# Kernel tuning notes

Measured on AMD Instinct MI355X. Metric: run time of the kernel, lower is better.

The kernel has to match this reference:

```python
import jax, jax.numpy as jnp
import numpy as np
import math

DIM = 896
NH = 8
HD = DIM // NH  # 112
B, T, KA_RAW, KT = 64, 8, 64, 512
KA = KA_RAW + 1  # adapter tokens + p conditioning token


def rope_cos_sin(L, hd):
    inv = 1.0 / (10000.0 ** (jnp.arange(0, hd, 2, dtype=jnp.float32) / hd))
    freqs = jnp.arange(L, dtype=jnp.float32)[:, None] * inv[None, :]  # (L, hd/2)
    emb = jnp.concatenate([freqs, freqs], axis=-1)  # (L, hd)
    return jnp.cos(emb), jnp.sin(emb)


def rotate_half(x):
    # interleaved rotation, faithful to the torch code
    x1 = x[..., ::2]
    x2 = x[..., 1::2]
    return jnp.stack((-x2, x1), axis=-1).reshape(x.shape)


def rope_apply(t, cos, sin):
    # cos/sin: (L, hd) broadcast over (B, H, L, hd)
    return t * cos + rotate_half(t) * sin


def heads(t):
    Bb, L, _ = t.shape
    return t.reshape(Bb, L, NH, HD).transpose(0, 2, 1, 3)  # (B, H, L, hd)


def setup_inputs() -> dict:
    key = jax.random.key(0)
    ks = jax.random.split(key, 32)
    s = 0.02
    d = {
        'x': jax.random.normal(ks[0], (B, T, DIM), jnp.float32),
        'h_a': jax.random.normal(ks[1], (B, KA_RAW, DIM), jnp.float32),
        'h_t': jax.random.normal(ks[2], (B, KT, DIM), jnp.float32),
        'p': jax.random.normal(ks[3], (B, 1, DIM), jnp.float32),
    }
    names = ['Wq', 'Wks', 'Wvs', 'Wka', 'Wva', 'Wkt', 'Wvt', 'Wo', 'Wf']
    for i, n in enumerate(names):
        d[n] = s * jax.random.normal(ks[4 + i], (DIM, DIM), jnp.float32)
        d['b' + n[1:]] = s * jax.random.normal(ks[16 + i], (DIM,), jnp.float32)
    d['gate'] = jnp.full((1,), 0.1, jnp.float32)  # nonzero so task branch is active
    d['ln_g'] = jnp.ones((DIM,), jnp.float32)
    d['ln_b'] = jnp.zeros((DIM,), jnp.float32)
    return d


def reference(x, h_a, h_t, p,
              Wq, bq, Wks, bks, Wvs, bvs, Wka, bka, Wva, bva,
              Wkt, bkt, Wvt, bvt, Wo, bo, Wf, bf,
              gate, ln_g, ln_b):
    ratio_g = jnp.tanh(gate)  # (1,)
    h_ad = jnp.concatenate([h_a, p], axis=1)  # (B, KA, C)

    q = heads(x @ Wq + bq)            # (B,H,T,hd)
    k_s = heads(x @ Wks + bks)
    v_s = heads(x @ Wvs + bvs)
    k_a = heads(h_ad @ Wka + bka)     # (B,H,KA,hd)
    v_a = heads(h_ad @ Wva + bva)
    k_t = heads(h_t @ Wkt + bkt)      # (B,H,KT,hd)
    v_t = heads(h_t @ Wvt + bvt)

    cos_m, sin_m = rope_cos_sin(T, HD)
    q = rope_apply(q, cos_m, sin_m)
    k_s = rope_apply(k_s, cos_m, sin_m)
    cos_a, sin_a = rope_cos_sin(KA, HD)
    k_a = rope_apply(k_a, cos_a, sin_a)
    cos_t, sin_t = rope_cos_sin(KT, HD)
    k_t = rope_apply(k_t, cos_t, sin_t)

    s_self = jnp.einsum('bhtd,bhkd->bhtk', q, k_s)
    s_ad = jnp.einsum('bhtd,bhkd->bhtk', q, k_a)
    s_task = jnp.einsum('bhtd,bhkd->bhtk', q, k_t) * ratio_g
    scores = jnp.concatenate([s_self, s_ad, s_task], axis=-1) / math.sqrt(HD)
    w = jax.nn.softmax(scores, axis=-1)  # (B,H,T,T+KA+KT)

    v = jnp.concatenate([v_s, v_a, v_t], axis=2)  # (B,H,T+KA+KT,hd)
    out = jnp.einsum('bhtk,bhkd->bhtd', w, v)
    out = out.transpose(0, 2, 1, 3).reshape(x.shape)  # (B,T,C)
    out = out @ Wo + bo

    y = out + x
    mu = jnp.mean(y, axis=-1, keepdims=True)
    var = jnp.var(y, axis=-1, keepdims=True)
    yn = (y - mu) / jnp.sqrt(var + 1e-5) * ln_g + ln_b
    return jax.nn.relu(yn @ Wf + bf)
```

## Files before the change

### kernel.cpp

```cpp
#include <hip/hip_runtime.h>
#include <hip/hip_bf16.h>
#include <math.h>

#define DIM 896
#define DD  (DIM * DIM)
#define NH 8
#define HD 112
#define BB 64
#define TT 8
#define KA 65
#define KAPAD 4224
#define KT 512
#define NKEYS (TT + KA + KT)

#define EPI_NONE  0
#define EPI_ROPE  1
#define EPI_RESID 2
#define EPI_RELU  3

#define NEG_L2_10K_OVER_56 (-0.2373327285062406f)

#ifndef __has_builtin
#define __has_builtin(x) 0
#endif
#if __has_builtin(__builtin_amdgcn_global_load_lds)
#define HAS_GLL 1
#else
#define HAS_GLL 0
#endif

typedef __attribute__((ext_vector_type(8))) short bf16x8_t;
typedef __attribute__((ext_vector_type(4))) float f32x4_t;

__device__ __forceinline__ short f2bf(float f) {
  unsigned u = __float_as_uint(f);
  u += 0x7fffu + ((u >> 16) & 1u);
  return (short)(u >> 16);
}
__device__ __forceinline__ float bf2f(short s) {
  return __uint_as_float(((unsigned)(unsigned short)s) << 16);
}
__device__ __forceinline__ unsigned cvt_pk_bf16(float lo, float hi) {
  unsigned r;
  asm("v_cvt_pk_bf16_f32 %0, %1, %2" : "=v"(r) : "v"(lo), "v"(hi));
  return r;
}

struct W9 { const float* w[9]; };

__global__ __launch_bounds__(256) void wtrans(W9 ws, short* __restrict__ Wt)
{
  __shared__ float t[32][33];
  const float* W = ws.w[blockIdx.z];
  short* dst = Wt + (size_t)blockIdx.z * DD;
  const int bx = blockIdx.x, by = blockIdx.y;
  const int tx = threadIdx.x & 31, ty = threadIdx.x >> 5;
#pragma unroll
  for (int i = 0; i < 4; ++i)
    t[ty + i * 8][tx] = W[(size_t)(by * 32 + ty + i * 8) * DIM + bx * 32 + tx];
  __syncthreads();
#pragma unroll
  for (int i = 0; i < 4; ++i)
    dst[(size_t)(bx * 32 + ty + i * 8) * DIM + by * 32 + tx] = f2bf(t[tx][ty + i * 8]);
}

__global__ __launch_bounds__(256) void build_had(
    const float* __restrict__ h_a, const float* __restrict__ p,
    short* __restrict__ had)
{
  const int i = blockIdx.x * 256 + threadIdx.x;
  const int total = KAPAD * DIM / 8;
  if (i >= total) return;
  const int c = (i % 112) * 8;
  const int row = i / 112;
  bf16x8_t o;
  if (row >= BB * KA) {
#pragma unroll
    for (int j = 0; j < 8; ++j) o[j] = 0;
  } else {
    const int b = row / KA, j = row % KA;
    const float* src = (j < KA - 1) ? h_a + ((size_t)b * (KA - 1) + j) * DIM + c
                                    : p + (size_t)b * DIM + c;
    const float4 a = *(const float4*)src;
    const float4 d = *(const float4*)(src + 4);
    o[0] = f2bf(a.x); o[1] = f2bf(a.y); o[2] = f2bf(a.z); o[3] = f2bf(a.w);
    o[4] = f2bf(d.x); o[5] = f2bf(d.y); o[6] = f2bf(d.z); o[7] = f2bf(d.w);
  }
  ((bf16x8_t*)had)[i] = o;
}

struct EpiCfg {
  const float* bias[3];
  float* outF[3];
  short* outB[3];
  const float* resid;
  int epi[3];
  int pos_mod[3];
  int row_off;
  int hm[3];
  int hm_L[3];
  int hm_ltot[3];
  int swz;
};

template <bool AF32>
__global__ __launch_bounds__(256) void gemm_bf16(
    const short* __restrict__ A, const float* __restrict__ Af,
    const short* __restrict__ Wt, EpiCfg cfg)
{
  __shared__ __align__(16) short As[128 * 32];
  __shared__ __align__(16) short Bs[128 * 32];
  const int tid = threadIdx.x;
  const int wave = tid >> 6, lane = tid & 63;

  int bx = blockIdx.x, by = blockIdx.y;
  if (cfg.swz) {
    const int nx = gridDim.x;
    const int bid = blockIdx.x + blockIdx.y * nx;
    const int xcd = bid & 7, ixd = bid >> 3;
    const int rpx = gridDim.y >> 3;
    bx = ixd % nx;
    by = xcd * rpx + ixd / nx;
  }
  const int sub = bx / 7;
  const int col0 = (bx % 7) * 128;
  const int row0 = by * 128;
  const int wm = wave >> 1, wn = wave & 1;
  const int lm = lane & 15, lq = lane >> 4;

  const int sm = lane >> 2, sk = (lane & 3) * 8;
  const short* Ag0 = A + (size_t)(row0 + wave * 32 + sm) * DIM + sk;
  const short* Ag1 = Ag0 + (size_t)16 * DIM;
  const short* Wg0 = Wt + (size_t)(sub * DIM + col0 + wave * 32 + sm) * DIM + sk;
  const short* Wg1 = Wg0 + (size_t)16 * DIM;

  const int am = tid >> 2, ako = (tid & 3) * 8;
  const float* af0 = nullptr;
  const float* af1 = nullptr;
  float4 c0a, c0b, c1a, c1b;
  if constexpr (AF32) {
    af0 = Af + (size_t)(row0 + am) * DIM + ako;
    af1 = Af + (size_t)(row0 + 64 + am) * DIM + ako;
    c0a = *(const float4*)(af0);
    c0b = *(const float4*)(af0 + 4);
    c1a = *(const float4*)(af1);
    c1b = *(const float4*)(af1 + 4);
  }

  f32x4_t acc[4][4];
#pragma unroll
  for (int i = 0; i < 4; ++i)
#pragma unroll
    for (int j = 0; j < 4; ++j) acc[i][j] = (f32x4_t){0.f, 0.f, 0.f, 0.f};

  for (int k0 = 0; k0 < DIM; k0 += 32) {
    __syncthreads();
    if constexpr (AF32) {
      const int kn = (k0 + 32 < DIM) ? (k0 + 32) : 0;
      const float4 n0a = *(const float4*)(af0 + kn);
      const float4 n0b = *(const float4*)(af0 + kn + 4);
      const float4 n1a = *(const float4*)(af1 + kn);
      const float4 n1b = *(const float4*)(af1 + kn + 4);
      uint4 w;
      w.x = cvt_pk_bf16(c0a.x, c0a.y);
      w.y = cvt_pk_bf16(c0a.z, c0a.w);
      w.z = cvt_pk_bf16(c0b.x, c0b.y);
      w.w = cvt_pk_bf16(c0b.z, c0b.w);
      *(uint4*)&As[tid * 8] = w;
      w.x = cvt_pk_bf16(c1a.x, c1a.y);
      w.y = cvt_pk_bf16(c1a.z, c1a.w);
      w.z = cvt_pk_bf16(c1b.x, c1b.y);
      w.w = cvt_pk_bf16(c1b.z, c1b.w);
      *(uint4*)&As[(tid + 256) * 8] = w;
      c0a = n0a; c0b = n0b; c1a = n1a; c1b = n1b;
    }
#if HAS_GLL
    if constexpr (!AF32) {
      __builtin_amdgcn_global_load_lds(
          (const __attribute__((address_space(1))) unsigned*)(Ag0 + k0),
          (__attribute__((address_space(3))) unsigned*)&As[(wave * 32) * 32], 16, 0, 0);
      __builtin_amdgcn_global_load_lds(
          (const __attribute__((address_space(1))) unsigned*)(Ag1 + k0),
          (__attribute__((address_space(3))) unsigned*)&As[(wave * 32 + 16) * 32], 16, 0, 0);
    }
    __builtin_amdgcn_global_load_lds(
        (const __attribute__((address_space(1))) unsigned*)(Wg0 + k0),
        (__attribute__((address_space(3))) unsigned*)&Bs[(wave * 32) * 32], 16, 0, 0);
    __builtin_amdgcn_global_load_lds(
        (const __attribute__((address_space(1))) unsigned*)(Wg1 + k0),
        (__attribute__((address_space(3))) unsigned*)&Bs[(wave * 32 + 16) * 32], 16, 0, 0);
#else
    {
      const int m = tid >> 1, kh = (tid & 1) * 16;
      if constexpr (!AF32) {
        *(bf16x8_t*)&As[m * 32 + kh] =
            *(const bf16x8_t*)(A + (size_t)(row0 + m) * DIM + k0 + kh);
        *(bf16x8_t*)&As[m * 32 + kh + 8] =
            *(const bf16x8_t*)(A + (size_t)(row0 + m) * DIM + k0 + kh + 8);
      }
      *(bf16x8_t*)&Bs[m * 32 + kh] =
          *(const bf16x8_t*)(Wt + (size_t)(sub * DIM + col0 + m) * DIM + k0 + kh);
      *(bf16x8_t*)&Bs[m * 32 + kh + 8] =
          *(const bf16x8_t*)(Wt + (size_t)(sub * DIM + col0 + m) * DIM + k0 + kh + 8);
    }
#endif
    __syncthreads();

    bf16x8_t af[4], bfr[4];
#pragma unroll
    for (int t = 0; t < 4; ++t)
      af[t] = *(const bf16x8_t*)&As[(wm * 64 + t * 16 + lm) * 32 + lq * 8];
#pragma unroll
    for (int t = 0; t < 4; ++t)
      bfr[t] = *(const bf16x8_t*)&Bs[(wn * 64 + t * 16 + lm) * 32 + lq * 8];
#pragma unroll
    for (int tm = 0; tm < 4; ++tm)
#pragma unroll
      for (int tn = 0; tn < 4; ++tn)
        acc[tm][tn] = __builtin_amdgcn_mfma_f32_16x16x32_bf16(
            af[tm], bfr[tn], acc[tm][tn], 0, 0, 0);
  }

  const float* bias = cfg.bias[sub];
  float* outF = cfg.outF[sub];
  short* outB = cfg.outB[sub];
  const int epi = cfg.epi[sub], pm = cfg.pos_mod[sub];
  const int hm = cfg.hm[sub];
  const int L = cfg.hm_L[sub], ltot = cfg.hm_ltot[sub];
  int gb[4][4], gl[4][4];
  if (hm) {
#pragma unroll
    for (int tm = 0; tm < 4; ++tm) {
      const int g = cfg.row_off + row0 + wm * 64 + tm * 16 + lq * 4;
      int bq2 = g / L;
      int l = g - bq2 * L;
#pragma unroll
      for (int r = 0; r < 4; ++r) {
        gb[tm][r] = bq2; gl[tm][r] = l;
        if (++l == L) { l = 0; ++bq2; }
      }
    }
  }
#pragma unroll
  for (int tn = 0; tn < 4; ++tn) {
    const int col = col0 + wn * 64 + tn * 16 + lm;
    const float bv = bias[col];
    int hcol = 0, dcol = 0;
    if (hm) { hcol = col / HD; dcol = col - hcol * HD; }
    float fr = 0.f, sgn = 0.f;
    if (epi == EPI_ROPE) {
      const int d0 = col % HD;
      fr = exp2f((float)(d0 % 56) * NEG_L2_10K_OVER_56);
      sgn = (d0 & 1) ? 1.f : -1.f;
    }
#pragma unroll
    for (int tm = 0; tm < 4; ++tm) {
#pragma unroll
      for (int r = 0; r < 4; ++r) {
        const int grow = cfg.row_off + row0 + wm * 64 + tm * 16 + lq * 4 + r;
        float v = acc[tm][tn][r] + bv;
        if (epi == EPI_ROPE) {
          const float prt = __shfl_xor(v, 1);
          const int pos = hm ? gl[tm][r] : (grow % pm);
          float s, c;
          __sincosf((float)pos * fr, &s, &c);
          v = v * c + sgn * prt * s;
        } else if (epi == EPI_RESID) {
          v += cfg.resid[(size_t)grow * DIM + col];
        } else if (epi == EPI_RELU) {
          v = fmaxf(v, 0.f);
        }
        if (hm) {
          if (gb[tm][r] < BB)
            outB[((size_t)(gb[tm][r] * NH + hcol) * ltot + gl[tm][r]) * HD + dcol] =
                f2bf(v);
        } else if (outB) {
          outB[(size_t)grow * DIM + col] = f2bf(v);
        } else {
          outF[(size_t)grow * DIM + col] = v;
        }
      }
    }
  }
}

#define SCP 10

__global__ __launch_bounds__(1024, 8) void attn_kernel(
    const short* __restrict__ q, const short* __restrict__ kall,
    const short* __restrict__ vall, const float* __restrict__ gate,
    short* __restrict__ out)
{
  __shared__ __align__(16) float qs[TT * HD];
  __shared__ __align__(16) float sc[NKEYS * SCP];
  __shared__ float red[TT * TT * HD];
  __shared__ float isum[TT];
  const int tid = threadIdx.x;
  const int bh = blockIdx.x;
  const float scale = 0.09449111825230681f;
  const float rg = tanhf(gate[0]);

  if (tid < TT * HD) qs[tid] = bf2f(q[(size_t)bh * (TT * HD) + tid]);
  __syncthreads();

  if (tid < NKEYS) {
    const int k = tid;
    const short* kp = kall + ((size_t)bh * NKEYS + k) * HD;
    float dot[TT] = {};
    for (int d8 = 0; d8 < HD; d8 += 8) {
      const bf16x8_t kv8 = *(const bf16x8_t*)(kp + d8);
      float kf[8];
#pragma unroll
      for (int j = 0; j < 8; ++j) kf[j] = bf2f(kv8[j]);
#pragma unroll
      for (int t = 0; t < TT; ++t) {
        const float4 qa = *(const float4*)&qs[t * HD + d8];
        const float4 qb4 = *(const float4*)&qs[t * HD + d8 + 4];
        dot[t] = fmaf(qa.x, kf[0], dot[t]);
        dot[t] = fmaf(qa.y, kf[1], dot[t]);
        dot[t] = fmaf(qa.z, kf[2], dot[t]);
        dot[t] = fmaf(qa.w, kf[3], dot[t]);
        dot[t] = fmaf(qb4.x, kf[4], dot[t]);
        dot[t] = fmaf(qb4.y, kf[5], dot[t]);
        dot[t] = fmaf(qb4.z, kf[6], dot[t]);
        dot[t] = fmaf(qb4.w, kf[7], dot[t]);
      }
    }
    const float s = (k >= TT + KA) ? scale * rg : scale;
#pragma unroll
    for (int t = 0; t < TT; ++t) sc[k * SCP + t] = dot[t] * s;
  }
  __syncthreads();

  const int wave = tid >> 6, lane = tid & 63;
  if (wave < TT) {
    const int t = wave;
    float m = -1e30f;
    for (int k = lane; k < NKEYS; k += 64) m = fmaxf(m, sc[k * SCP + t]);
#pragma unroll
    for (int o = 32; o >= 1; o >>= 1) m = fmaxf(m, __shfl_xor(m, o));
    float sum = 0.f;
    for (int k = lane; k < NKEYS; k += 64) {
      const float e = expf(sc[k * SCP + t] - m);
      sc[k * SCP + t] = e;
      sum += e;
    }
#pragma unroll
    for (int o = 32; o >= 1; o >>= 1) sum += __shfl_xor(sum, o);
    if (lane == 0) isum[t] = 1.f / sum;
  }
  __syncthreads();

  if (tid < TT * HD) {
    const int g = tid / HD, d = tid - (tid / HD) * HD;
    const int kb = (g * NKEYS) / TT, ke = ((g + 1) * NKEYS) / TT;
    const short* vp = vall + (size_t)bh * (NKEYS * HD) + d;
    float acc[TT] = {};
    for (int k = kb; k < ke; ++k) {
      const float vv = bf2f(vp[(size_t)k * HD]);
      const float2 s0 = *(const float2*)&sc[k * SCP];
      const float2 s1 = *(const float2*)&sc[k * SCP + 2];
      const float2 s2 = *(const float2*)&sc[k * SCP + 4];
      const float2 s3 = *(const float2*)&sc[k * SCP + 6];
      acc[0] = fmaf(s0.x, vv, acc[0]);
      acc[1] = fmaf(s0.y, vv, acc[1]);
      acc[2] = fmaf(s1.x, vv, acc[2]);
      acc[3] = fmaf(s1.y, vv, acc[3]);
      acc[4] = fmaf(s2.x, vv, acc[4]);
      acc[5] = fmaf(s2.y, vv, acc[5]);
      acc[6] = fmaf(s3.x, vv, acc[6]);
      acc[7] = fmaf(s3.y, vv, acc[7]);
    }
#pragma unroll
    for (int t = 0; t < TT; ++t) red[(g * TT + t) * HD + d] = acc[t];
  }
  __syncthreads();

  if (tid < TT * HD) {
    const int t = tid / HD, d = tid - (tid / HD) * HD;
    float a = 0.f;
#pragma unroll
    for (int g = 0; g < TT; ++g) a += red[(g * TT + t) * HD + d];
    out[((size_t)(bh >> 3) * TT + t) * DIM + (bh & 7) * HD + d] = f2bf(a * isum[t]);
  }
}

__global__ __launch_bounds__(256) void ln_kernel(
    const float* __restrict__ y, const float* __restrict__ g,
    const float* __restrict__ beta, short* __restrict__ yn)
{
  __shared__ float s1[4], s2[4];
  const int r = blockIdx.x, tid = threadIdx.x;
  const float* row = y + (size_t)r * DIM;
  float sum = 0.f, sq = 0.f;
  for (int c = tid; c < DIM; c += 256) {
    const float v = row[c];
    sum += v;
    sq = fmaf(v, v, sq);
  }
#pragma unroll
  for (int o = 32; o >= 1; o >>= 1) {
    sum += __shfl_xor(sum, o);
    sq  += __shfl_xor(sq, o);
  }
  const int wave = tid >> 6, lane = tid & 63;
  if (lane == 0) { s1[wave] = sum; s2[wave] = sq; }
  __syncthreads();
  sum = s1[0] + s1[1] + s1[2] + s1[3];
  sq  = s2[0] + s2[1] + s2[2] + s2[3];
  const float mu = sum / DIM;
  const float var = sq / DIM - mu * mu;
  const float rstd = 1.f / sqrtf(var + 1e-5f);
  for (int c = tid; c < DIM; c += 256)
    yn[(size_t)r * DIM + c] = f2bf((row[c] - mu) * rstd * g[c] + beta[c]);
}

extern "C" void kernel_launch(void* const* d_in, const int* in_sizes, int n_in,
                              void* d_out, int out_size, void* d_ws, size_t ws_size,
                              hipStream_t stream)
{
  const float* x   = (const float*)d_in[0];
  const float* h_a = (const float*)d_in[1];
  const float* h_t = (const float*)d_in[2];
  const float* p   = (const float*)d_in[3];
  const float* Wq  = (const float*)d_in[4];  const float* bq  = (const float*)d_in[5];
  const float* Wks = (const float*)d_in[6];  const float* bks = (const float*)d_in[7];
  const float* Wvs = (const float*)d_in[8];  const float* bvs = (const float*)d_in[9];
  const float* Wka = (const float*)d_in[10]; const float* bka = (const float*)d_in[11];
  const float* Wva = (const float*)d_in[12]; const float* bva = (const float*)d_in[13];
  const float* Wkt = (const float*)d_in[14]; const float* bkt = (const float*)d_in[15];
  const float* Wvt = (const float*)d_in[16]; const float* bvt = (const float*)d_in[17];
  const float* Wo  = (const float*)d_in[18]; const float* bo  = (const float*)d_in[19];
  const float* Wf  = (const float*)d_in[20]; const float* bf_ = (const float*)d_in[21];
  const float* gate = (const float*)d_in[22];
  const float* ln_g = (const float*)d_in[23];
  const float* ln_b = (const float*)d_in[24];

  const size_t SZ_HAD = (size_t)KAPAD * DIM * 2;
  const size_t SZ_SM  = (size_t)BB * TT * DIM * 2;
  const size_t SZ_KV  = (size_t)BB * NH * NKEYS * HD * 2;
  const size_t SZ_WT  = (size_t)9 * DD * 2;
  const size_t needed = SZ_HAD + SZ_SM * 3 + SZ_KV * 2 + SZ_WT
                        + (size_t)BB * TT * DIM * 4;
  if (ws_size < needed) return;

  char* wsp = (char*)d_ws;
  short* hadb = (short*)wsp; wsp += SZ_HAD;
  short* qb   = (short*)wsp; wsp += SZ_SM;
  short* kall = (short*)wsp; wsp += SZ_KV;
  short* vall = (short*)wsp; wsp += SZ_KV;
  short* WtA  = (short*)wsp; wsp += SZ_WT;
  short* attn_outb = (short*)wsp; wsp += SZ_SM;
  float* yb   = (float*)wsp; wsp += (size_t)BB * TT * DIM * 4;
  short* ynb  = (short*)wsp; wsp += SZ_SM;

  dim3 blk(256);

  W9 w9; const float* Ws[9] = {Wq, Wks, Wvs, Wka, Wva, Wkt, Wvt, Wo, Wf};
  for (int i = 0; i < 9; ++i) w9.w[i] = Ws[i];
  wtrans<<<dim3(28, 28, 9), blk, 0, stream>>>(w9, WtA);

  build_had<<<(KAPAD * DIM / 8 + 255) / 256, blk, 0, stream>>>(h_a, p, hadb);

  {
    EpiCfg c = {};
    c.bias[0] = bq;  c.outB[0] = qb;   c.epi[0] = EPI_ROPE; c.pos_mod[0] = TT;
    c.hm[0] = 1; c.hm_L[0] = TT; c.hm_ltot[0] = TT;
    c.bias[1] = bks; c.outB[1] = kall; c.epi[1] = EPI_ROPE; c.pos_mod[1] = TT;
    c.hm[1] = 1; c.hm_L[1] = TT; c.hm_ltot[1] = NKEYS;
    c.bias[2] = bvs; c.outB[2] = vall; c.epi[2] = EPI_NONE; c.pos_mod[2] = 1;
    c.hm[2] = 1; c.hm_L[2] = TT; c.hm_ltot[2] = NKEYS;
    gemm_bf16<true><<<dim3(21, BB * TT / 128), blk, 0, stream>>>(nullptr, x, WtA, c);
  }
  {
    EpiCfg c = {};
    c.bias[0] = bka; c.outB[0] = kall + (size_t)TT * HD; c.epi[0] = EPI_ROPE;
    c.pos_mod[0] = KA; c.hm[0] = 1; c.hm_L[0] = KA; c.hm_ltot[0] = NKEYS;
    c.bias[1] = bva; c.outB[1] = vall + (size_t)TT * HD; c.epi[1] = EPI_NONE;
    c.pos_mod[1] = 1; c.hm[1] = 1; c.hm_L[1] = KA; c.hm_ltot[1] = NKEYS;
    gemm_bf16<false><<<dim3(14, KAPAD / 128), blk, 0, stream>>>(
        hadb, nullptr, WtA + (size_t)3 * DD, c);
  }
  {
    EpiCfg c = {};
    c.bias[0] = bkt; c.outB[0] = kall + (size_t)(TT + KA) * HD; c.epi[0] = EPI_ROPE;
    c.pos_mod[0] = KT; c.hm[0] = 1; c.hm_L[0] = KT; c.hm_ltot[0] = NKEYS;
    c.bias[1] = bvt; c.outB[1] = vall + (size_t)(TT + KA) * HD; c.epi[1] = EPI_NONE;
    c.pos_mod[1] = 1; c.hm[1] = 1; c.hm_L[1] = KT; c.hm_ltot[1] = NKEYS;
    c.row_off = 0;
    c.swz = 1;
    gemm_bf16<true><<<dim3(14, BB * KT / 128), blk, 0, stream>>>(
        nullptr, h_t, WtA + (size_t)5 * DD, c);
  }

  attn_kernel<<<BB * NH, dim3(1024), 0, stream>>>(qb, kall, vall, gate, attn_outb);

  {
    EpiCfg c = {};
    c.bias[0] = bo; c.outF[0] = yb; c.epi[0] = EPI_RESID; c.pos_mod[0] = 1;
    c.resid = x;
    gemm_bf16<false><<<dim3(7, BB * TT / 128), blk, 0, stream>>>(
        attn_outb, nullptr, WtA + (size_t)7 * DD, c);
  }
  ln_kernel<<<BB * TT, blk, 0, stream>>>(yb, ln_g, ln_b, ynb);
  {
    EpiCfg c = {};
    c.bias[0] = bf_; c.outF[0] = (float*)d_out; c.epi[0] = EPI_RELU; c.pos_mod[0] = 1;
    gemm_bf16<false><<<dim3(7, BB * TT / 128), blk, 0, stream>>>(
        ynb, nullptr, WtA + (size_t)8 * DD, c);
  }
}
```

Before: 799.6 us.

## Double-buffer GEMM LDS tiles so global loads overlap MFMA compute

The GEMM main loop now uses two LDS buffers for A and B. Each phase issues loads for the next K slice into the other buffer while running MFMAs on the current one, so only one barrier per 32-wide K step remains instead of two. The fp32 A path loads the next slice into registers before the MFMAs and converts and stores it afterwards. This doubles LDS usage to 32 KB per block, which may reduce occupancy.

```diff
diff --git a/kernel.cpp b/kernel.cpp
--- a/kernel.cpp
+++ b/kernel.cpp
@@ -44,6 +44,15 @@
   unsigned r;
   asm("v_cvt_pk_bf16_f32 %0, %1, %2" : "=v"(r) : "v"(lo), "v"(hi));
   return r;
+}
+__device__ __forceinline__ void gll16(const short* g, short* lbase, int lane) {
+#if HAS_GLL
+  __builtin_amdgcn_global_load_lds(
+      (const __attribute__((address_space(1))) unsigned*)g,
+      (__attribute__((address_space(3))) unsigned*)lbase, 16, 0, 0);
+#else
+  *(bf16x8_t*)(lbase + lane * 8) = *(const bf16x8_t*)g;
+#endif
 }
 
 struct W9 { const float* w[9]; };
@@ -108,8 +117,10 @@
     const short* __restrict__ A, const float* __restrict__ Af,
     const short* __restrict__ Wt, EpiCfg cfg)
 {
-  __shared__ __align__(16) short As[128 * 32];
-  __shared__ __align__(16) short Bs[128 * 32];
+  __shared__ __align__(16) short AsA[128 * 32];
+  __shared__ __align__(16) short AsB[128 * 32];
+  __shared__ __align__(16) short BsA[128 * 32];
+  __shared__ __align__(16) short BsB[128 * 32];
   const int tid = threadIdx.x;
   const int wave = tid >> 6, lane = tid & 63;
 
@@ -137,14 +148,9 @@
   const int am = tid >> 2, ako = (tid & 3) * 8;
   const float* af0 = nullptr;
   const float* af1 = nullptr;
-  float4 c0a, c0b, c1a, c1b;
   if constexpr (AF32) {
     af0 = Af + (size_t)(row0 + am) * DIM + ako;
-    af1 = Af + (size_t)(row0 + 64 + am) * DIM + ako;
-    c0a = *(const float4*)(af0);
-    c0b = *(const float4*)(af0 + 4);
-    c1a = *(const float4*)(af1);
-    c1b = *(const float4*)(af1 + 4);
+    af1 = af0 + (size_t)64 * DIM;
   }
 
   f32x4_t acc[4][4];
@@ -153,73 +159,74 @@
 #pragma unroll
     for (int j = 0; j < 4; ++j) acc[i][j] = (f32x4_t){0.f, 0.f, 0.f, 0.f};
 
-  for (int k0 = 0; k0 < DIM; k0 += 32) {
-    __syncthreads();
-    if constexpr (AF32) {
-      const int kn = (k0 + 32 < DIM) ? (k0 + 32) : 0;
-      const float4 n0a = *(const float4*)(af0 + kn);
-      const float4 n0b = *(const float4*)(af0 + kn + 4);
-      const float4 n1a = *(const float4*)(af1 + kn);
-      const float4 n1b = *(const float4*)(af1 + kn + 4);
-      uint4 w;
-      w.x = cvt_pk_bf16(c0a.x, c0a.y);
-      w.y = cvt_pk_bf16(c0a.z, c0a.w);
-      w.z = cvt_pk_bf16(c0b.x, c0b.y);
-      w.w = cvt_pk_bf16(c0b.z, c0b.w);
-      *(uint4*)&As[tid * 8] = w;
-      w.x = cvt_pk_bf16(c1a.x, c1a.y);
-      w.y = cvt_pk_bf16(c1a.z, c1a.w);
-      w.z = cvt_pk_bf16(c1b.x, c1b.y);
-      w.w = cvt_pk_bf16(c1b.z, c1b.w);
-      *(uint4*)&As[(tid + 256) * 8] = w;
-      c0a = n0a; c0b = n0b; c1a = n1a; c1b = n1b;
-    }
-#if HAS_GLL
-    if constexpr (!AF32) {
-      __builtin_amdgcn_global_load_lds(
-          (const __attribute__((address_space(1))) unsigned*)(Ag0 + k0),
-          (__attribute__((address_space(3))) unsigned*)&As[(wave * 32) * 32], 16, 0, 0);
-      __builtin_amdgcn_global_load_lds(
-          (const __attribute__((address_space(1))) unsigned*)(Ag1 + k0),
-          (__attribute__((address_space(3))) unsigned*)&As[(wave * 32 + 16) * 32], 16, 0, 0);
-    }
-    __builtin_amdgcn_global_load_lds(
-        (const __attribute__((address_space(1))) unsigned*)(Wg0 + k0),
-        (__attribute__((address_space(3))) unsigned*)&Bs[(wave * 32) * 32], 16, 0, 0);
-    __builtin_amdgcn_global_load_lds(
-        (const __attribute__((address_space(1))) unsigned*)(Wg1 + k0),
-        (__attribute__((address_space(3))) unsigned*)&Bs[(wave * 32 + 16) * 32], 16, 0, 0);
-#else
-    {
-      const int m = tid >> 1, kh = (tid & 1) * 16;
-      if constexpr (!AF32) {
-        *(bf16x8_t*)&As[m * 32 + kh] =
-            *(const bf16x8_t*)(A + (size_t)(row0 + m) * DIM + k0 + kh);
-        *(bf16x8_t*)&As[m * 32 + kh + 8] =
-            *(const bf16x8_t*)(A + (size_t)(row0 + m) * DIM + k0 + kh + 8);
-      }
-      *(bf16x8_t*)&Bs[m * 32 + kh] =
-          *(const bf16x8_t*)(Wt + (size_t)(sub * DIM + col0 + m) * DIM + k0 + kh);
-      *(bf16x8_t*)&Bs[m * 32 + kh + 8] =
-          *(const bf16x8_t*)(Wt + (size_t)(sub * DIM + col0 + m) * DIM + k0 + kh + 8);
-    }
-#endif
-    __syncthreads();
-
-    bf16x8_t af[4], bfr[4];
-#pragma unroll
-    for (int t = 0; t < 4; ++t)
-      af[t] = *(const bf16x8_t*)&As[(wm * 64 + t * 16 + lm) * 32 + lq * 8];
-#pragma unroll
-    for (int t = 0; t < 4; ++t)
-      bfr[t] = *(const bf16x8_t*)&Bs[(wn * 64 + t * 16 + lm) * 32 + lq * 8];
-#pragma unroll
-    for (int tm = 0; tm < 4; ++tm)
-#pragma unroll
-      for (int tn = 0; tn < 4; ++tn)
-        acc[tm][tn] = __builtin_amdgcn_mfma_f32_16x16x32_bf16(
-            af[tm], bfr[tn], acc[tm][tn], 0, 0, 0);
-  }
+  if constexpr (AF32) {
+    const float4 p0a = *(const float4*)(af0);
+    const float4 p0b = *(const float4*)(af0 + 4);
+    const float4 p1a = *(const float4*)(af1);
+    const float4 p1b = *(const float4*)(af1 + 4);
+    uint4 w;
+    w.x = cvt_pk_bf16(p0a.x, p0a.y); w.y = cvt_pk_bf16(p0a.z, p0a.w);
+    w.z = cvt_pk_bf16(p0b.x, p0b.y); w.w = cvt_pk_bf16(p0b.z, p0b.w);
+    *(uint4*)&AsA[tid * 8] = w;
+    w.x = cvt_pk_bf16(p1a.x, p1a.y); w.y = cvt_pk_bf16(p1a.z, p1a.w);
+    w.z = cvt_pk_bf16(p1b.x, p1b.y); w.w = cvt_pk_bf16(p1b.z, p1b.w);
+    *(uint4*)&AsA[(tid + 256) * 8] = w;
+  } else {
+    gll16(Ag0, &AsA[(wave * 32) * 32], lane);
+    gll16(Ag1, &AsA[(wave * 32 + 16) * 32], lane);
+  }
+  gll16(Wg0, &BsA[(wave * 32) * 32], lane);
+  gll16(Wg1, &BsA[(wave * 32 + 16) * 32], lane);
+  __syncthreads();
+
+#define GEMM_PHASE(AsX, BsX, AsY, BsY, kn, doStage)                            \
+  {                                                                            \
+    float4 n0a, n0b, n1a, n1b;                                                 \
+    if (doStage) {                                                             \
+      if constexpr (AF32) {                                                    \
+        n0a = *(const float4*)(af0 + (kn));                                    \
+        n0b = *(const float4*)(af0 + (kn) + 4);                                \
+        n1a = *(const float4*)(af1 + (kn));                                    \
+        n1b = *(const float4*)(af1 + (kn) + 4);                                \
+      } else {                                                                 \
+        gll16(Ag0 + (kn), &AsY[(wave * 32) * 32], lane);                       \
+        gll16(Ag1 + (kn), &AsY[(wave * 32 + 16) * 32], lane);                  \
+      }                                                                        \
+      gll16(Wg0 + (kn), &BsY[(wave * 32) * 32], lane);                         \
+      gll16(Wg1 + (kn), &BsY[(wave * 32 + 16) * 32], lane);                    \
+    }                                                                          \
+    bf16x8_t afr[4], bfr[4];                                                   \
+    _Pragma("unroll")                                                          \
+    for (int t = 0; t < 4; ++t)                                                \
+      afr[t] = *(const bf16x8_t*)&AsX[(wm * 64 + t * 16 + lm) * 32 + lq * 8];  \
+    _Pragma("unroll")                                                          \
+    for (int t = 0; t < 4; ++t)                                                \
+      bfr[t] = *(const bf16x8_t*)&BsX[(wn * 64 + t * 16 + lm) * 32 + lq * 8];  \
+    _Pragma("unroll")                                                          \
+    for (int tm = 0; tm < 4; ++tm)                                             \
+      _Pragma("unroll")                                                        \
+      for (int tn = 0; tn < 4; ++tn)                                           \
+        acc[tm][tn] = __builtin_amdgcn_mfma_f32_16x16x32_bf16(                 \
+            afr[tm], bfr[tn], acc[tm][tn], 0, 0, 0);                           \
+    if constexpr (AF32) {                                                      \
+      if (doStage) {                                                           \
+        uint4 w;                                                               \
+        w.x = cvt_pk_bf16(n0a.x, n0a.y); w.y = cvt_pk_bf16(n0a.z, n0a.w);      \
+        w.z = cvt_pk_bf16(n0b.x, n0b.y); w.w = cvt_pk_bf16(n0b.z, n0b.w);      \
+        *(uint4*)&AsY[tid * 8] = w;                                            \
+        w.x = cvt_pk_bf16(n1a.x, n1a.y); w.y = cvt_pk_bf16(n1a.z, n1a.w);      \
+        w.z = cvt_pk_bf16(n1b.x, n1b.y); w.w = cvt_pk_bf16(n1b.z, n1b.w);      \
+        *(uint4*)&AsY[(tid + 256) * 8] = w;                                    \
+      }                                                                        \
+    }                                                                          \
+    __syncthreads();                                                           \
+  }
+
+  for (int k0 = 0; k0 < DIM; k0 += 64) {
+    GEMM_PHASE(AsA, BsA, AsB, BsB, k0 + 32, true);
+    GEMM_PHASE(AsB, BsB, AsA, BsA, k0 + 64, (k0 + 64) < DIM);
+  }
+#undef GEMM_PHASE
 
   const float* bias = cfg.bias[sub];
   float* outF = cfg.outF[sub];
```

New measurement: 883.6 us. +10.5%, slower.

## Merge QKV projection GEMMs into one launch and fuse LayerNorm into FFN GEMM

Applied to the files above, without the earlier changes.

The three projection GEMMs (self, adapter, task) are combined into a single grid-partitioned kernel that picks its input and weights per block, removing two launches and the tails between them. The LayerNorm kernel is removed: the FFN GEMM computes per-row mean and rstd from the fp32 residual output and applies the normalization while converting A tiles to bf16. The cost is a runtime af32 branch instead of a template parameter, and each FFN block redundantly recomputes row statistics for its 128 rows across 7 column blocks.

```diff
diff --git a/kernel.cpp b/kernel.cpp
--- a/kernel.cpp
+++ b/kernel.cpp
@@ -13,6 +13,10 @@
 #define KT 512
 #define NKEYS (TT + KA + KT)
 
+#define NS_BLK 84
+#define NA_BLK 462
+#define NT_BLK 3584
+
 #define EPI_NONE  0
 #define EPI_ROPE  1
 #define EPI_RESID 2
@@ -44,6 +48,15 @@
   unsigned r;
   asm("v_cvt_pk_bf16_f32 %0, %1, %2" : "=v"(r) : "v"(lo), "v"(hi));
   return r;
+}
+__device__ __forceinline__ void gll16(const short* g, short* lbase, int lane) {
+#if HAS_GLL
+  __builtin_amdgcn_global_load_lds(
+      (const __attribute__((address_space(1))) unsigned*)g,
+      (__attribute__((address_space(3))) unsigned*)lbase, 16, 0, 0);
+#else
+  *(bf16x8_t*)(lbase + lane * 8) = *(const bf16x8_t*)g;
+#endif
 }
 
 struct W9 { const float* w[9]; };
@@ -100,28 +113,17 @@
   int hm[3];
   int hm_L[3];
   int hm_ltot[3];
-  int swz;
 };
 
-template <bool AF32>
-__global__ __launch_bounds__(256) void gemm_bf16(
-    const short* __restrict__ A, const float* __restrict__ Af,
-    const short* __restrict__ Wt, EpiCfg cfg)
-{
-  __shared__ __align__(16) short As[128 * 32];
-  __shared__ __align__(16) short Bs[128 * 32];
+__device__ __forceinline__ void gemm_body(
+    short* As, short* Bs,
+    const short* A, const float* Af, const short* Wt,
+    const EpiCfg& cfg, int bx, int by, bool af32,
+    bool doLN, float mu0, float rs0, float mu1, float rs1,
+    const float* lngam, const float* lnbet)
+{
   const int tid = threadIdx.x;
   const int wave = tid >> 6, lane = tid & 63;
-
-  int bx = blockIdx.x, by = blockIdx.y;
-  if (cfg.swz) {
-    const int nx = gridDim.x;
-    const int bid = blockIdx.x + blockIdx.y * nx;
-    const int xcd = bid & 7, ixd = bid >> 3;
-    const int rpx = gridDim.y >> 3;
-    bx = ixd % nx;
-    by = xcd * rpx + ixd / nx;
-  }
   const int sub = bx / 7;
   const int col0 = (bx % 7) * 128;
   const int row0 = by * 128;
@@ -129,22 +131,25 @@
   const int lm = lane & 15, lq = lane >> 4;
 
   const int sm = lane >> 2, sk = (lane & 3) * 8;
-  const short* Ag0 = A + (size_t)(row0 + wave * 32 + sm) * DIM + sk;
-  const short* Ag1 = Ag0 + (size_t)16 * DIM;
   const short* Wg0 = Wt + (size_t)(sub * DIM + col0 + wave * 32 + sm) * DIM + sk;
   const short* Wg1 = Wg0 + (size_t)16 * DIM;
 
-  const int am = tid >> 2, ako = (tid & 3) * 8;
+  const short* Ag0 = nullptr;
+  const short* Ag1 = nullptr;
   const float* af0 = nullptr;
   const float* af1 = nullptr;
+  const int am = tid >> 2, ako = (tid & 3) * 8;
   float4 c0a, c0b, c1a, c1b;
-  if constexpr (AF32) {
+  if (af32) {
     af0 = Af + (size_t)(row0 + am) * DIM + ako;
-    af1 = Af + (size_t)(row0 + 64 + am) * DIM + ako;
+    af1 = af0 + (size_t)64 * DIM;
     c0a = *(const float4*)(af0);
     c0b = *(const float4*)(af0 + 4);
     c1a = *(const float4*)(af1);
     c1b = *(const float4*)(af1 + 4);
+  } else {
+    Ag0 = A + (size_t)(row0 + wave * 32 + sm) * DIM + sk;
+    Ag1 = Ag0 + (size_t)16 * DIM;
   }
 
   f32x4_t acc[4][4];
@@ -155,61 +160,43 @@
 
   for (int k0 = 0; k0 < DIM; k0 += 32) {
     __syncthreads();
-    if constexpr (AF32) {
+    if (af32) {
       const int kn = (k0 + 32 < DIM) ? (k0 + 32) : 0;
       const float4 n0a = *(const float4*)(af0 + kn);
       const float4 n0b = *(const float4*)(af0 + kn + 4);
       const float4 n1a = *(const float4*)(af1 + kn);
       const float4 n1b = *(const float4*)(af1 + kn + 4);
+      float e0[8] = {c0a.x, c0a.y, c0a.z, c0a.w, c0b.x, c0b.y, c0b.z, c0b.w};
+      float e1[8] = {c1a.x, c1a.y, c1a.z, c1a.w, c1b.x, c1b.y, c1b.z, c1b.w};
+      if (doLN) {
+#pragma unroll
+        for (int j = 0; j < 8; ++j) {
+          const int k = k0 + ako + j;
+          const float g = lngam[k], b = lnbet[k];
+          e0[j] = (e0[j] - mu0) * rs0 * g + b;
+          e1[j] = (e1[j] - mu1) * rs1 * g + b;
+        }
+      }
       uint4 w;
-      w.x = cvt_pk_bf16(c0a.x, c0a.y);
-      w.y = cvt_pk_bf16(c0a.z, c0a.w);
-      w.z = cvt_pk_bf16(c0b.x, c0b.y);
-      w.w = cvt_pk_bf16(c0b.z, c0b.w);
+      w.x = cvt_pk_bf16(e0[0], e0[1]); w.y = cvt_pk_bf16(e0[2], e0[3]);
+      w.z = cvt_pk_bf16(e0[4], e0[5]); w.w = cvt_pk_bf16(e0[6], e0[7]);
       *(uint4*)&As[tid * 8] = w;
-      w.x = cvt_pk_bf16(c1a.x, c1a.y);
-      w.y = cvt_pk_bf16(c1a.z, c1a.w);
-      w.z = cvt_pk_bf16(c1b.x, c1b.y);
-      w.w = cvt_pk_bf16(c1b.z, c1b.w);
+      w.x = cvt_pk_bf16(e1[0], e1[1]); w.y = cvt_pk_bf16(e1[2], e1[3]);
+      w.z = cvt_pk_bf16(e1[4], e1[5]); w.w = cvt_pk_bf16(e1[6], e1[7]);
       *(uint4*)&As[(tid + 256) * 8] = w;
       c0a = n0a; c0b = n0b; c1a = n1a; c1b = n1b;
-    }
-#if HAS_GLL
-    if constexpr (!AF32) {
-      __builtin_amdgcn_global_load_lds(
-          (const __attribute__((address_space(1))) unsigned*)(Ag0 + k0),
-          (__attribute__((address_space(3))) unsigned*)&As[(wave * 32) * 32], 16, 0, 0);
-      __builtin_amdgcn_global_load_lds(
-          (const __attribute__((address_space(1))) unsigned*)(Ag1 + k0),
-          (__attribute__((address_space(3))) unsigned*)&As[(wave * 32 + 16) * 32], 16, 0, 0);
-    }
-    __builtin_amdgcn_global_load_lds(
-        (const __attribute__((address_space(1))) unsigned*)(Wg0 + k0),
-        (__attribute__((address_space(3))) unsigned*)&Bs[(wave * 32) * 32], 16, 0, 0);
-    __builtin_amdgcn_global_load_lds(
-        (const __attribute__((address_space(1))) unsigned*)(Wg1 + k0),
-        (__attribute__((address_space(3))) unsigned*)&Bs[(wave * 32 + 16) * 32], 16, 0, 0);
-#else
-    {
-      const int m = tid >> 1, kh = (tid & 1) * 16;
-      if constexpr (!AF32) {
-        *(bf16x8_t*)&As[m * 32 + kh] =
-            *(const bf16x8_t*)(A + (size_t)(row0 + m) * DIM + k0 + kh);
-        *(bf16x8_t*)&As[m * 32 + kh + 8] =
-            *(const bf16x8_t*)(A + (size_t)(row0 + m) * DIM + k0 + kh + 8);
-      }
-      *(bf16x8_t*)&Bs[m * 32 + kh] =
-          *(const bf16x8_t*)(Wt + (size_t)(sub * DIM + col0 + m) * DIM + k0 + kh);
-      *(bf16x8_t*)&Bs[m * 32 + kh + 8] =
-          *(const bf16x8_t*)(Wt + (size_t)(sub * DIM + col0 + m) * DIM + k0 + kh + 8);
-    }
-#endif
+    } else {
+      gll16(Ag0 + k0, &As[(wave * 32) * 32], lane);
+      gll16(Ag1 + k0, &As[(wave * 32 + 16) * 32], lane);
+    }
+    gll16(Wg0 + k0, &Bs[(wave * 32) * 32], lane);
+    gll16(Wg1 + k0, &Bs[(wave * 32 + 16) * 32], lane);
     __syncthreads();
 
-    bf16x8_t af[4], bfr[4];
+    bf16x8_t afr[4], bfr[4];
 #pragma unroll
     for (int t = 0; t < 4; ++t)
-      af[t] = *(const bf16x8_t*)&As[(wm * 64 + t * 16 + lm) * 32 + lq * 8];
+      afr[t] = *(const bf16x8_t*)&As[(wm * 64 + t * 16 + lm) * 32 + lq * 8];
 #pragma unroll
     for (int t = 0; t < 4; ++t)
       bfr[t] = *(const bf16x8_t*)&Bs[(wn * 64 + t * 16 + lm) * 32 + lq * 8];
@@ -218,7 +205,7 @@
 #pragma unroll
       for (int tn = 0; tn < 4; ++tn)
         acc[tm][tn] = __builtin_amdgcn_mfma_f32_16x16x32_bf16(
-            af[tm], bfr[tn], acc[tm][tn], 0, 0, 0);
+            afr[tm], bfr[tn], acc[tm][tn], 0, 0, 0);
   }
 
   const float* bias = cfg.bias[sub];
@@ -284,6 +271,80 @@
   }
 }
 
+__global__ __launch_bounds__(256) void qkv_gemm(
+    const float* __restrict__ x, const short* __restrict__ hadb,
+    const float* __restrict__ h_t, const short* __restrict__ Wt,
+    EpiCfg cS, EpiCfg cA, EpiCfg cT)
+{
+  __shared__ __align__(16) short As[128 * 32];
+  __shared__ __align__(16) short Bs[128 * 32];
+  const int b = blockIdx.x;
+  int bx, by;
+  const short* A = nullptr;
+  const float* Af = nullptr;
+  const short* W;
+  if (b < NS_BLK) {
+    bx = b % 21; by = b / 21;
+    Af = x; W = Wt;
+  } else if (b < NS_BLK + NA_BLK) {
+    const int t = b - NS_BLK;
+    bx = t % 14; by = t / 14;
+    A = hadb; W = Wt + (size_t)3 * DD;
+  } else {
+    const int t = b - NS_BLK - NA_BLK;
+    const int xcd = t & 7, ixd = t >> 3;
+    bx = ixd % 14; by = xcd * 32 + ixd / 14;
+    Af = h_t; W = Wt + (size_t)5 * DD;
+  }
+  const EpiCfg& c = (b < NS_BLK) ? cS : (b < NS_BLK + NA_BLK ? cA : cT);
+  gemm_body(As, Bs, A, Af, W, c, bx, by, Af != nullptr,
+            false, 0.f, 0.f, 0.f, 0.f, nullptr, nullptr);
+}
+
+__global__ __launch_bounds__(256) void gemm_one(
+    const short* __restrict__ A, const short* __restrict__ Wt, EpiCfg cfg)
+{
+  __shared__ __align__(16) short As[128 * 32];
+  __shared__ __align__(16) short Bs[128 * 32];
+  gemm_body(As, Bs, A, nullptr, Wt, cfg, blockIdx.x, blockIdx.y, false,
+            false, 0.f, 0.f, 0.f, 0.f, nullptr, nullptr);
+}
+
+__global__ __launch_bounds__(256) void gemm_ffn(
+    const float* __restrict__ Y, const float* __restrict__ lng,
+    const float* __restrict__ lnb, const short* __restrict__ Wt, EpiCfg cfg)
+{
+  __shared__ __align__(16) short As[128 * 32];
+  __shared__ __align__(16) short Bs[128 * 32];
+  __shared__ float glds[DIM], blds[DIM];
+  __shared__ float smu[128], srs[128];
+  const int tid = threadIdx.x;
+  const int row0 = blockIdx.y * 128;
+  for (int i = tid; i < DIM; i += 256) { glds[i] = lng[i]; blds[i] = lnb[i]; }
+  {
+    const int r = tid >> 1, h = tid & 1;
+    const float* rp = Y + (size_t)(row0 + r) * DIM + h * 448;
+    float s = 0.f, q = 0.f;
+    for (int i = 0; i < 448; i += 4) {
+      const float4 v = *(const float4*)(rp + i);
+      s += v.x + v.y + v.z + v.w;
+      q = fmaf(v.x, v.x, fmaf(v.y, v.y, fmaf(v.z, v.z, fmaf(v.w, v.w, q))));
+    }
+    s += __shfl_xor(s, 1);
+    q += __shfl_xor(q, 1);
+    if (h == 0) {
+      const float mu = s * (1.f / DIM);
+      const float var = q * (1.f / DIM) - mu * mu;
+      smu[r] = mu;
+      srs[r] = 1.f / sqrtf(var + 1e-5f);
+    }
+  }
+  __syncthreads();
+  const int am = tid >> 2;
+  gemm_body(As, Bs, nullptr, Y, Wt, cfg, blockIdx.x, blockIdx.y, true,
+            true, smu[am], srs[am], smu[am + 64], srs[am + 64], glds, blds);
+}
+
 #define SCP 10
 
 __global__ __launch_bounds__(1024, 8) void attn_kernel(
@@ -385,36 +446,6 @@
   }
 }
 
-__global__ __launch_bounds__(256) void ln_kernel(
-    const float* __restrict__ y, const float* __restrict__ g,
-    const float* __restrict__ beta, short* __restrict__ yn)
-{
-  __shared__ float s1[4], s2[4];
-  const int r = blockIdx.x, tid = threadIdx.x;
-  const float* row = y + (size_t)r * DIM;
-  float sum = 0.f, sq = 0.f;
-  for (int c = tid; c < DIM; c += 256) {
-    const float v = row[c];
-    sum += v;
-    sq = fmaf(v, v, sq);
-  }
-#pragma unroll
-  for (int o = 32; o >= 1; o >>= 1) {
-    sum += __shfl_xor(sum, o);
-    sq  += __shfl_xor(sq, o);
-  }
-  const int wave = tid >> 6, lane = tid & 63;
-  if (lane == 0) { s1[wave] = sum; s2[wave] = sq; }
-  __syncthreads();
-  sum = s1[0] + s1[1] + s1[2] + s1[3];
-  sq  = s2[0] + s2[1] + s2[2] + s2[3];
-  const float mu = sum / DIM;
-  const float var = sq / DIM - mu * mu;
-  const float rstd = 1.f / sqrtf(var + 1e-5f);
-  for (int c = tid; c < DIM; c += 256)
-    yn[(size_t)r * DIM + c] = f2bf((row[c] - mu) * rstd * g[c] + beta[c]);
-}
-
 extern "C" void kernel_launch(void* const* d_in, const int* in_sizes, int n_in,
                               void* d_out, int out_size, void* d_ws, size_t ws_size,
                               hipStream_t stream)
@@ -440,7 +471,7 @@
   const size_t SZ_SM  = (size_t)BB * TT * DIM * 2;
   const size_t SZ_KV  = (size_t)BB * NH * NKEYS * HD * 2;
   const size_t SZ_WT  = (size_t)9 * DD * 2;
-  const size_t needed = SZ_HAD + SZ_SM * 3 + SZ_KV * 2 + SZ_WT
+  const size_t needed = SZ_HAD + SZ_SM * 2 + SZ_KV * 2 + SZ_WT
                         + (size_t)BB * TT * DIM * 4;
   if (ws_size < needed) return;
 
@@ -452,7 +483,6 @@
   short* WtA  = (short*)wsp; wsp += SZ_WT;
   short* attn_outb = (short*)wsp; wsp += SZ_SM;
   float* yb   = (float*)wsp; wsp += (size_t)BB * TT * DIM * 4;
-  short* ynb  = (short*)wsp; wsp += SZ_SM;
 
   dim3 blk(256);
 
@@ -462,36 +492,28 @@
 
   build_had<<<(KAPAD * DIM / 8 + 255) / 256, blk, 0, stream>>>(h_a, p, hadb);
 
-  {
-    EpiCfg c = {};
-    c.bias[0] = bq;  c.outB[0] = qb;   c.epi[0] = EPI_ROPE; c.pos_mod[0] = TT;
-    c.hm[0] = 1; c.hm_L[0] = TT; c.hm_ltot[0] = TT;
-    c.bias[1] = bks; c.outB[1] = kall; c.epi[1] = EPI_ROPE; c.pos_mod[1] = TT;
-    c.hm[1] = 1; c.hm_L[1] = TT; c.hm_ltot[1] = NKEYS;
-    c.bias[2] = bvs; c.outB[2] = vall; c.epi[2] = EPI_NONE; c.pos_mod[2] = 1;
-    c.hm[2] = 1; c.hm_L[2] = TT; c.hm_ltot[2] = NKEYS;
-    gemm_bf16<true><<<dim3(21, BB * TT / 128), blk, 0, stream>>>(nullptr, x, WtA, c);
-  }
-  {
-    EpiCfg c = {};
-    c.bias[0] = bka; c.outB[0] = kall + (size_t)TT * HD; c.epi[0] = EPI_ROPE;
-    c.pos_mod[0] = KA; c.hm[0] = 1; c.hm_L[0] = KA; c.hm_ltot[0] = NKEYS;
-    c.bias[1] = bva; c.outB[1] = vall + (size_t)TT * HD; c.epi[1] = EPI_NONE;
-    c.pos_mod[1] = 1; c.hm[1] = 1; c.hm_L[1] = KA; c.hm_ltot[1] = NKEYS;
-    gemm_bf16<false><<<dim3(14, KAPAD / 128), blk, 0, stream>>>(
-        hadb, nullptr, WtA + (size_t)3 * DD, c);
-  }
-  {
-    EpiCfg c = {};
-    c.bias[0] = bkt; c.outB[0] = kall + (size_t)(TT + KA) * HD; c.epi[0] = EPI_ROPE;
-    c.pos_mod[0] = KT; c.hm[0] = 1; c.hm_L[0] = KT; c.hm_ltot[0] = NKEYS;
-    c.bias[1] = bvt; c.outB[1] = vall + (size_t)(TT + KA) * HD; c.epi[1] = EPI_NONE;
-    c.pos_mod[1] = 1; c.hm[1] = 1; c.hm_L[1] = KT; c.hm_ltot[1] = NKEYS;
-    c.row_off = 0;
-    c.swz = 1;
-    gemm_bf16<true><<<dim3(14, BB * KT / 128), blk, 0, stream>>>(
-        nullptr, h_t, WtA + (size_t)5 * DD, c);
-  }
+  EpiCfg cS = {};
+  cS.bias[0] = bq;  cS.outB[0] = qb;   cS.epi[0] = EPI_ROPE; cS.pos_mod[0] = TT;
+  cS.hm[0] = 1; cS.hm_L[0] = TT; cS.hm_ltot[0] = TT;
+  cS.bias[1] = bks; cS.outB[1] = kall; cS.epi[1] = EPI_ROPE; cS.pos_mod[1] = TT;
+  cS.hm[1] = 1; cS.hm_L[1] = TT; cS.hm_ltot[1] = NKEYS;
+  cS.bias[2] = bvs; cS.outB[2] = vall; cS.epi[2] = EPI_NONE; cS.pos_mod[2] = 1;
+  cS.hm[2] = 1; cS.hm_L[2] = TT; cS.hm_ltot[2] = NKEYS;
+
+  EpiCfg cA = {};
+  cA.bias[0] = bka; cA.outB[0] = kall + (size_t)TT * HD; cA.epi[0] = EPI_ROPE;
+  cA.pos_mod[0] = KA; cA.hm[0] = 1; cA.hm_L[0] = KA; cA.hm_ltot[0] = NKEYS;
+  cA.bias[1] = bva; cA.outB[1] = vall + (size_t)TT * HD; cA.epi[1] = EPI_NONE;
+  cA.pos_mod[1] = 1; cA.hm[1] = 1; cA.hm_L[1] = KA; cA.hm_ltot[1] = NKEYS;
+
+  EpiCfg cT = {};
+  cT.bias[0] = bkt; cT.outB[0] = kall + (size_t)(TT + KA) * HD; cT.epi[0] = EPI_ROPE;
+  cT.pos_mod[0] = KT; cT.hm[0] = 1; cT.hm_L[0] = KT; cT.hm_ltot[0] = NKEYS;
+  cT.bias[1] = bvt; cT.outB[1] = vall + (size_t)(TT + KA) * HD; cT.epi[1] = EPI_NONE;
+  cT.pos_mod[1] = 1; cT.hm[1] = 1; cT.hm_L[1] = KT; cT.hm_ltot[1] = NKEYS;
+
+  qkv_gemm<<<dim3(NS_BLK + NA_BLK + NT_BLK), blk, 0, stream>>>(
+      x, hadb, h_t, WtA, cS, cA, cT);
 
   attn_kernel<<<BB * NH, dim3(1024), 0, stream>>>(qb, kall, vall, gate, attn_outb);
 
@@ -499,14 +521,13 @@
     EpiCfg c = {};
     c.bias[0] = bo; c.outF[0] = yb; c.epi[0] = EPI_RESID; c.pos_mod[0] = 1;
     c.resid = x;
-    gemm_bf16<false><<<dim3(7, BB * TT / 128), blk, 0, stream>>>(
-        attn_outb, nullptr, WtA + (size_t)7 * DD, c);
-  }
-  ln_kernel<<<BB * TT, blk, 0, stream>>>(yb, ln_g, ln_b, ynb);
+    gemm_one<<<dim3(7, BB * TT / 128), blk, 0, stream>>>(
+        attn_outb, WtA + (size_t)7 * DD, c);
+  }
   {
     EpiCfg c = {};
     c.bias[0] = bf_; c.outF[0] = (float*)d_out; c.epi[0] = EPI_RELU; c.pos_mod[0] = 1;
-    gemm_bf16<false><<<dim3(7, BB * TT / 128), blk, 0, stream>>>(
-        ynb, nullptr, WtA + (size_t)8 * DD, c);
-  }
-}
+    gemm_ffn<<<dim3(7, BB * TT / 128), blk, 0, stream>>>(
+        yb, ln_g, ln_b, WtA + (size_t)8 * DD, c);
+  }
+}
```

After: 868.5 us. +8.6%, slower.
